# Kernel optimization log

Hardware: AMD Instinct MI355X
Metric: run time of the kernel (lower is better)

The kernel has to match this reference:

```python
import jax, jax.numpy as jnp
import numpy as np

B, S, D = 4, 2048, 1024  # batch, seq_len, d_emb (even for Givens pairs)


def givens_rotate(r, x):
    """Apply 2x2 Givens block rotations defined by r [D] to x [..., D]."""
    g = r.reshape(-1, 2)
    g = g / jnp.linalg.norm(g, axis=-1, keepdims=True)  # normalize (cos, sin) pairs
    xp = x.reshape(x.shape[:-1] + (x.shape[-1] // 2, 2))
    c, s = g[:, 0], g[:, 1]
    y0 = c * xp[..., 0] - s * xp[..., 1]
    y1 = c * xp[..., 1] + s * xp[..., 0]
    return jnp.stack([y0, y1], axis=-1).reshape(x.shape)


def setup_inputs() -> dict:
    key = jax.random.key(0)
    k1, k2 = jax.random.split(key, 2)
    Q = jax.random.normal(k1, (B, S, D), dtype=jnp.float32)
    # QKV_rotation.weight ~ U(-1, 1) per original init (before the identity overwrite)
    rot_w = jax.random.uniform(k2, (3, D), dtype=jnp.float32, minval=-1.0, maxval=1.0)
    scale = jnp.array([np.sqrt(D)], dtype=jnp.float32)
    bias = jnp.zeros((), dtype=jnp.float32)
    return {"Q": Q, "rot_w": rot_w, "scale": scale, "bias": bias}


def reference(Q, rot_w, scale, bias):
    # Givens-rotation 'projections' for q/k/v
    q = givens_rotate(rot_w[0], Q)
    k = givens_rotate(rot_w[1], Q)
    v = givens_rotate(rot_w[2], Q)
    # prepend zero time coordinate -> points on the Lorentz model ambient space
    zeros = jnp.zeros(Q.shape[:-1] + (1,), Q.dtype)
    q = jnp.concatenate([zeros, q], axis=-1)[:, None]  # [B,1,S,D+1]
    k = jnp.concatenate([zeros, k], axis=-1)[:, None]
    v = jnp.concatenate([zeros, v], axis=-1)[:, None]
    # Lorentz signature (-, +, +, ...)
    sgn = jnp.concatenate([-jnp.ones((1,), Q.dtype), jnp.ones((q.shape[-1] - 1,), Q.dtype)])
    # cinner(q, k): time-negated inner product -> scores [B,1,S,S]
    cin = jnp.einsum('bhqd,bhkd->bhqk', q * sgn, k)
    attn = jax.nn.softmax((2.0 + 2.0 * cin) / scale + bias, axis=-1)
    # Lorentz mid-point: weighted sum normalized by sqrt(|<m,m>_L|)
    ave = jnp.einsum('bhqk,bhkd->bhqd', attn, v)
    inner = jnp.sum(ave * ave * sgn, axis=-1, keepdims=True)
    denom = jnp.sqrt(jnp.clip(jnp.abs(inner), 1e-8, None))
    out = (ave / denom)[:, 0]  # [B,S,D+1]
    return out[..., 1:]  # drop time coordinate -> [B,S,D]
```

## Files before the change

kernel.cpp:

```cpp
#include <hip/hip_runtime.h>

typedef _Float16 h16;
typedef _Float16 half8 __attribute__((ext_vector_type(8)));
typedef float floatx4 __attribute__((ext_vector_type(4)));

static constexpr int Bb_ = 4, S_ = 2048, D_ = 1024;

static __device__ __forceinline__ void gl_lds16(const void* g, void* l) {
  __builtin_amdgcn_global_load_lds(
      (const __attribute__((address_space(1))) unsigned int*)g,
      (__attribute__((address_space(3))) unsigned int*)l, 16, 0, 0);
}

static __device__ __forceinline__ void rot_pair(float q0, float q1, float a0,
                                                float a1, float b0, float b1,
                                                float c0, float c1, float& y0,
                                                float& y1, float& v0,
                                                float& v1) {
  float iqk = rsqrtf((a0 * a0 + a1 * a1) * (b0 * b0 + b1 * b1));
  float cc = (a0 * b0 + a1 * b1) * iqk;
  float ss = (a0 * b1 - a1 * b0) * iqk;
  y0 = cc * q0 - ss * q1;
  y1 = cc * q1 + ss * q0;
  float iv = rsqrtf(c0 * c0 + c1 * c1);
  float cv = c0 * iv, sv = c1 * iv;
  v0 = cv * q0 - sv * q1;
  v1 = cv * q1 + sv * q0;
}

__global__ __launch_bounds__(256) void k_prep_t(
    const float* __restrict__ Q, const float* __restrict__ rot,
    h16* __restrict__ Qh, h16* __restrict__ Kh, h16* __restrict__ VhT,
    float* __restrict__ pss, unsigned int* __restrict__ flags) {
  __shared__ __align__(16) h16 tile[64][64];
  int d0 = blockIdx.x * 64, s0 = blockIdx.y * 64, b = blockIdx.z;
  int t = threadIdx.x;
  int bl = blockIdx.x + 16 * (blockIdx.y + 32 * blockIdx.z);
  if (flags && bl == 0 && t < 32) flags[t] = 0u;
  if (pss && t < 4) pss[bl * 4 + t] = 0.f;
  const float* Qb = Q + ((size_t)b * S_ + s0) * D_ + d0;
  h16* Qhb = Qh + ((size_t)b * S_ + s0) * D_ + d0;
  h16* Khb = Kh + ((size_t)b * S_ + s0) * D_ + d0;
#pragma unroll
  for (int i = 0; i < 2; ++i) {
    int c = t + 256 * i;
    int row = c >> 3;
    int col = (c & 7) * 8;
    float4 qa = *(const float4*)&Qb[(size_t)row * D_ + col];
    float4 qb = *(const float4*)&Qb[(size_t)row * D_ + col + 4];
    int dg = (d0 + col) >> 2;
    float4 r0a = ((const float4*)rot)[dg];
    float4 r0b = ((const float4*)rot)[dg + 1];
    float4 r1a = ((const float4*)rot)[D_ / 4 + dg];
    float4 r1b = ((const float4*)rot)[D_ / 4 + dg + 1];
    float4 r2a = ((const float4*)rot)[2 * D_ / 4 + dg];
    float4 r2b = ((const float4*)rot)[2 * D_ / 4 + dg + 1];
    float y0, y1, y2, y3, y4, y5, y6, y7;
    float v0, v1, v2, v3, v4, v5, v6, v7;
    rot_pair(qa.x, qa.y, r0a.x, r0a.y, r1a.x, r1a.y, r2a.x, r2a.y, y0, y1, v0, v1);
    rot_pair(qa.z, qa.w, r0a.z, r0a.w, r1a.z, r1a.w, r2a.z, r2a.w, y2, y3, v2, v3);
    rot_pair(qb.x, qb.y, r0b.x, r0b.y, r1b.x, r1b.y, r2b.x, r2b.y, y4, y5, v4, v5);
    rot_pair(qb.z, qb.w, r0b.z, r0b.w, r1b.z, r1b.w, r2b.z, r2b.w, y6, y7, v6, v7);
    half8 qh = {(h16)qa.x, (h16)qa.y, (h16)qa.z, (h16)qa.w,
                (h16)qb.x, (h16)qb.y, (h16)qb.z, (h16)qb.w};
    half8 kh = {(h16)y0, (h16)y1, (h16)y2, (h16)y3,
                (h16)y4, (h16)y5, (h16)y6, (h16)y7};
    half8 vh = {(h16)v0, (h16)v1, (h16)v2, (h16)v3,
                (h16)v4, (h16)v5, (h16)v6, (h16)v7};
    *(half8*)&Qhb[(size_t)row * D_ + col] = qh;
    *(half8*)&Khb[(size_t)row * D_ + col] = kh;
    int pcol = col ^ ((row >> 3) << 3);
    *(half8*)&tile[row][pcol] = vh;
  }
  __syncthreads();
  h16* dst = VhT + ((size_t)b * D_ + d0) * S_ + s0;
#pragma unroll
  for (int i = 0; i < 2; ++i) {
    int c = t + 256 * i;
    int drow = c >> 3;
    int sc = (c & 7) * 8;
    int xr = sc;
    half8 v;
#pragma unroll
    for (int j = 0; j < 8; ++j) v[j] = tile[sc + j][drow ^ xr];
    *(half8*)&dst[(size_t)drow * S_ + sc] = v;
  }
}

#define G_FENCE asm volatile("" ::: "memory")
#define G_BAR                     \
  do {                            \
    G_FENCE;                      \
    __builtin_amdgcn_s_barrier(); \
    G_FENCE;                      \
  } while (0)

template <int NF, bool OUT16>
__global__ __launch_bounds__(512, 2) void k_gemm8(
    const char* __restrict__ A, int a_pitch, unsigned long long a_batch,
    const char* __restrict__ Bt, int b_pitch, unsigned long long b_batch,
    void* __restrict__ C, int c_pitch, unsigned long long c_batch, int Kdim,
    const float* __restrict__ scale_p, float* __restrict__ pss,
    unsigned int* __restrict__ flags) {
  constexpr int BNR = NF * 64;
  constexpr int JQ = NF / 2;
  __shared__ __align__(16) h16 As[2][2][256 * 32];
  __shared__ __align__(16) h16 Bs[2][2][BNR * 32];
  const int t = threadIdx.x;
  const int lane = t & 63;
  const int w = t >> 6;
  const int wm = (w >> 2) * 128;
  const int wn = (w & 3) * (NF * 16);
  const int id = blockIdx.x + 8 * (blockIdx.y + 8 * blockIdx.z);
  const int L = (id & 7) * 32 + (id >> 3);
  const int tm = L & 7, tn = (L >> 3) & 7, tz = L >> 6;
  const int grp = tz * 8 + tm;
  const char* Ab = A + (unsigned long long)tz * a_batch +
                   (unsigned long long)(tm * 256) * (unsigned long long)a_pitch;
  const char* Bb = Bt + (unsigned long long)tz * b_batch +
                   (unsigned long long)(tn * BNR) * (unsigned long long)b_pitch;
  const int srow = t >> 2;
  const int scol = ((t & 3) ^ ((t >> 3) & 3)) << 4;
  const int lds_o = t * 16;
  const int mrow = lane & 15, kc = lane >> 4;
  const int koff = (kc ^ ((mrow >> 1) & 3)) << 3;
  const int NT = Kdim >> 6;

#define SG_A(bf, kt, hm)                                                  \
  do {                                                                    \
    const char* sp_ = Ab +                                                \
                      (unsigned long long)(srow + (hm) * 128) * a_pitch + \
                      (kt) * 128 + scol;                                  \
    gl_lds16(sp_, (char*)&As[bf][0][(hm) * 128 * 32] + lds_o);            \
    gl_lds16(sp_ + 64, (char*)&As[bf][1][(hm) * 128 * 32] + lds_o);       \
  } while (0)
#define SG_B(bf, kt, hm)                                                  \
  do {                                                                    \
    const char* sp_ = Bb +                                                \
                      (unsigned long long)(srow + (hm) * 128) * b_pitch + \
                      (kt) * 128 + scol;                                  \
    gl_lds16(sp_, (char*)&Bs[bf][0][(hm) * 128 * 32] + lds_o);            \
    gl_lds16(sp_ + 64, (char*)&Bs[bf][1][(hm) * 128 * 32] + lds_o);       \
  } while (0)

  half8 ar0[4][2], ar1[4][2], br0[JQ][2], br1[JQ][2];
  floatx4 acc[8][NF];
#pragma unroll
  for (int i = 0; i < 8; ++i)
#pragma unroll
    for (int j = 0; j < NF; ++j) acc[i][j] = (floatx4){0.f, 0.f, 0.f, 0.f};

#define LDA_(bf, mh, DST)                                                \
  do {                                                                   \
    _Pragma("unroll") for (int i_ = 0; i_ < 4; ++i_) {                   \
      DST[i_][0] = *(const half8*)&As[bf][0]                             \
                       [(wm + ((mh) * 4 + i_) * 16 + mrow) * 32 + koff]; \
      DST[i_][1] = *(const half8*)&As[bf][1]                             \
                       [(wm + ((mh) * 4 + i_) * 16 + mrow) * 32 + koff]; \
    }                                                                    \
  } while (0)
#define LDB_(bf, nh, DST)                                                \
  do {                                                                   \
    _Pragma("unroll") for (int j_ = 0; j_ < JQ; ++j_) {                  \
      DST[j_][0] = *(const half8*)&Bs[bf][0]                             \
                       [(wn + ((nh)*JQ + j_) * 16 + mrow) * 32 + koff];  \
      DST[j_][1] = *(const half8*)&Bs[bf][1]                             \
                       [(wn + ((nh)*JQ + j_) * 16 + mrow) * 32 + koff];  \
    }                                                                    \
  } while (0)
#define QUAD(mh, nh, AF, BF)                                                 \
  do {                                                                       \
    __builtin_amdgcn_s_setprio(1);                                           \
    _Pragma("unroll") for (int i_ = 0; i_ < 4; ++i_)                         \
        _Pragma("unroll") for (int j_ = 0; j_ < JQ; ++j_) {                  \
      acc[(mh) * 4 + i_][(nh)*JQ + j_] =                                     \
          __builtin_amdgcn_mfma_f32_16x16x32_f16(                            \
              AF[i_][0], BF[j_][0], acc[(mh) * 4 + i_][(nh)*JQ + j_], 0, 0,  \
              0);                                                            \
      acc[(mh) * 4 + i_][(nh)*JQ + j_] =                                     \
          __builtin_amdgcn_mfma_f32_16x16x32_f16(                            \
              AF[i_][1], BF[j_][1], acc[(mh) * 4 + i_][(nh)*JQ + j_], 0, 0,  \
              0);                                                            \
    }                                                                        \
    __builtin_amdgcn_s_setprio(0);                                           \
  } while (0)

  SG_A(0, 0, 0);
  SG_A(0, 0, 1);
  SG_B(0, 0, 0);
  if constexpr (NF == 4) SG_B(0, 0, 1);
  SG_B(1, 1, 0);
  if constexpr (NF == 4) SG_B(1, 1, 1);
  SG_A(1, 1, 0);
  if constexpr (NF == 4)
    asm volatile("s_waitcnt vmcnt(6)" ::: "memory");
  else
    asm volatile("s_waitcnt vmcnt(4)" ::: "memory");
  G_BAR;
  LDA_(0, 0, ar0);
  LDB_(0, 0, br0);

#define TILE_(bf, nb, u)                                   \
  do {                                                     \
    const int k1_ = ((u) + 1 < NT) ? (u) + 1 : NT - 1;     \
    const int k2_ = ((u) + 2 < NT) ? (u) + 2 : NT - 1;     \
                                                   \
    SG_A(nb, k1_, 1);                                      \
    G_BAR;                                                 \
    LDB_(bf, 1, br1);                                      \
    QUAD(0, 0, ar0, br0);                                  \
                                                   \
    G_BAR;                                                 \
    LDA_(bf, 1, ar1);                                      \
    QUAD(0, 1, ar0, br1);                                  \
                                                   \
    SG_B(bf, k2_, 0);                                      \
    G_BAR;                                                 \
    QUAD(1, 0, ar1, br0);                                  \
                                                   \
    if constexpr (NF == 4) SG_B(bf, k2_, 1);               \
    SG_A(bf, k2_, 0);                                      \
    if constexpr (NF == 4)                                 \
      asm volatile("s_waitcnt vmcnt(6)" ::: "memory");     \
    else                                                   \
      asm volatile("s_waitcnt vmcnt(4)" ::: "memory");     \
    G_BAR;                                                 \
    LDA_(nb, 0, ar0);  \
    LDB_(nb, 0, br0);                                      \
    QUAD(1, 1, ar1, br1);                                  \
  } while (0)

  for (int u = 0; u < NT; u += 2) {
    TILE_(0, 1, u);
    TILE_(1, 0, u + 1);
  }
  asm volatile("s_waitcnt vmcnt(0)" ::: "memory");

  const int m0 = tm * 256 + wm;
  const int n0 = tn * BNR + wn;
  const int ccol = lane & 15;
  const int rq = (lane >> 4) * 4;
  if constexpr (OUT16) {
    const float aexp = 2.0f / scale_p[0];
    h16* Cb = (h16*)C + (unsigned long long)tz * c_batch;
#pragma unroll
    for (int i = 0; i < 8; ++i)
#pragma unroll
      for (int j = 0; j < NF; ++j)
#pragma unroll
        for (int r = 0; r < 4; ++r)
          Cb[(unsigned long long)(m0 + i * 16 + rq + r) * c_pitch +
             (n0 + j * 16 + ccol)] = (h16)__expf(acc[i][j][r] * aexp - 8.0f);
  } else {
    float* Cb = (float*)C + (unsigned long long)tz * c_batch;
    if (pss) {
      __syncthreads();
      float* wsum = (float*)&As[0][0][0];
      float* finv = wsum + 4 * 256;
      float part[8][4];
#pragma unroll
      for (int i = 0; i < 8; ++i)
#pragma unroll
        for (int r = 0; r < 4; ++r) {
          float s = acc[i][0][r] * acc[i][0][r];
          if constexpr (NF > 1) s += acc[i][1][r] * acc[i][1][r];
#pragma unroll
          for (int m = 1; m < 16; m <<= 1) s += __shfl_xor(s, m);
          part[i][r] = s;
        }
      if ((lane & 15) == 0) {
#pragma unroll
        for (int i = 0; i < 8; ++i)
#pragma unroll
          for (int r = 0; r < 4; ++r)
            wsum[(w & 3) * 256 + wm + i * 16 + rq + r] = part[i][r];
      }
      __syncthreads();
      if (t < 256) {
        float s = wsum[t] + wsum[256 + t] + wsum[512 + t] + wsum[768 + t];
        __hip_atomic_fetch_add(&pss[(unsigned)grp * 256 + t], s,
                               __ATOMIC_RELAXED, __HIP_MEMORY_SCOPE_AGENT);
      }
      __syncthreads();
      if (t == 0) {
        __hip_atomic_fetch_add(&flags[grp], 1u, __ATOMIC_ACQ_REL,
                               __HIP_MEMORY_SCOPE_AGENT);
        while (__hip_atomic_load(&flags[grp], __ATOMIC_ACQUIRE,
                                 __HIP_MEMORY_SCOPE_AGENT) < 8u)
          __builtin_amdgcn_s_sleep(2);
      }
      __syncthreads();
      if (t < 256) {
        float ss2 = __hip_atomic_load(&pss[(unsigned)grp * 256 + t],
                                      __ATOMIC_RELAXED,
                                      __HIP_MEMORY_SCOPE_AGENT);
        finv[t] = rsqrtf(fmaxf(ss2, 1e-30f));
      }
      __syncthreads();
#pragma unroll
      for (int i = 0; i < 8; ++i) {
#pragma unroll
        for (int r = 0; r < 4; ++r) {
          const float f = finv[wm + i * 16 + rq + r];
#pragma unroll
          for (int j = 0; j < NF; ++j)
            Cb[(unsigned long long)(m0 + i * 16 + rq + r) * c_pitch +
               (n0 + j * 16 + ccol)] = acc[i][j][r] * f;
        }
      }
    } else {
#pragma unroll
      for (int i = 0; i < 8; ++i)
#pragma unroll
        for (int j = 0; j < NF; ++j)
#pragma unroll
          for (int r = 0; r < 4; ++r)
            Cb[(unsigned long long)(m0 + i * 16 + rq + r) * c_pitch +
               (n0 + j * 16 + ccol)] = acc[i][j][r];
    }
  }
#undef TILE_
#undef QUAD
#undef LDB_
#undef LDA_
#undef SG_B
#undef SG_A
}

__global__ __launch_bounds__(256) void k_epilogue(float* __restrict__ O) {
  int wv = threadIdx.x >> 6, ln = threadIdx.x & 63;
  int row = blockIdx.x * 4 + wv;
  float* base = O + (size_t)row * D_;
  float4 u[4];
#pragma unroll
  for (int r = 0; r < 4; ++r) u[r] = ((const float4*)base)[ln + 64 * r];
  float ss = 0.f;
#pragma unroll
  for (int r = 0; r < 4; ++r)
    ss += u[r].x * u[r].x + u[r].y * u[r].y + u[r].z * u[r].z + u[r].w * u[r].w;
#pragma unroll
  for (int off = 32; off; off >>= 1) ss += __shfl_xor(ss, off);
  float f = rsqrtf(fmaxf(ss, 1e-30f));
#pragma unroll
  for (int r = 0; r < 4; ++r) {
    float4 o;
    o.x = u[r].x * f;
    o.y = u[r].y * f;
    o.z = u[r].z * f;
    o.w = u[r].w * f;
    ((float4*)base)[ln + 64 * r] = o;
  }
}

extern "C" void kernel_launch(void* const* d_in, const int* in_sizes, int n_in,
                              void* d_out, int out_size, void* d_ws, size_t ws_size,
                              hipStream_t stream) {
  const float* Q = (const float*)d_in[0];
  const float* rot = (const float*)d_in[1];
  const float* scale = (const float*)d_in[2];
  float* O = (float*)d_out;
  char* ws = (char*)d_ws;
  const size_t MB = 1024ull * 1024ull;
  h16* Qh = (h16*)(ws);
  h16* Kh = (h16*)(ws + 16 * MB);
  h16* VhT = (h16*)(ws + 32 * MB);
  h16* Sl = (h16*)(ws + 48 * MB);
  float* pss = (float*)(ws + 80 * MB);
  unsigned int* flags = (unsigned int*)(ws + 80 * MB + 32 * 1024);
  const bool fused = ws_size >= 80 * MB + 32 * 1024 + 128;
  if (!fused) {
    pss = nullptr;
    flags = nullptr;
  }

  k_prep_t<<<dim3(D_ / 64, S_ / 64, Bb_), 256, 0, stream>>>(Q, rot, Qh, Kh,
                                                            VhT, pss, flags);
  k_gemm8<4, true><<<dim3(8, 8, 4), 512, 0, stream>>>(
      (const char*)Qh, D_ * 2, (unsigned long long)S_ * D_ * 2,
      (const char*)Kh, D_ * 2, (unsigned long long)S_ * D_ * 2,
      (void*)Sl, S_, (unsigned long long)S_ * S_, D_, scale, nullptr, nullptr);
  k_gemm8<2, false><<<dim3(8, 8, 4), 512, 0, stream>>>(
      (const char*)Sl, S_ * 2, (unsigned long long)S_ * S_ * 2,
      (const char*)VhT, S_ * 2, (unsigned long long)D_ * S_ * 2,
      (void*)O, D_, (unsigned long long)S_ * D_, S_, nullptr, pss, flags);
  if (!fused) k_epilogue<<<dim3(Bb_ * S_ / 4), 256, 0, stream>>>(O);
}
```

Before: 177.5 us.

## Halve GEMM block to 4 waves, each computing double-width output tile

```diff
diff --git a/kernel.cpp b/kernel.cpp
--- a/kernel.cpp
+++ b/kernel.cpp
@@ -96,21 +96,21 @@
   } while (0)
 
 template <int NF, bool OUT16>
-__global__ __launch_bounds__(512, 2) void k_gemm8(
+__global__ __launch_bounds__(256, 1) void k_gemm8(
     const char* __restrict__ A, int a_pitch, unsigned long long a_batch,
     const char* __restrict__ Bt, int b_pitch, unsigned long long b_batch,
     void* __restrict__ C, int c_pitch, unsigned long long c_batch, int Kdim,
     const float* __restrict__ scale_p, float* __restrict__ pss,
     unsigned int* __restrict__ flags) {
   constexpr int BNR = NF * 64;
-  constexpr int JQ = NF / 2;
+  constexpr int NW = NF * 2;
   __shared__ __align__(16) h16 As[2][2][256 * 32];
   __shared__ __align__(16) h16 Bs[2][2][BNR * 32];
   const int t = threadIdx.x;
   const int lane = t & 63;
   const int w = t >> 6;
-  const int wm = (w >> 2) * 128;
-  const int wn = (w & 3) * (NF * 16);
+  const int wm = (w >> 1) * 128;
+  const int wn = (w & 1) * (NF * 32);
   const int id = blockIdx.x + 8 * (blockIdx.y + 8 * blockIdx.z);
   const int L = (id & 7) * 32 + (id >> 3);
   const int tm = L & 7, tn = (L >> 3) & 7, tz = L >> 6;
@@ -119,36 +119,47 @@
                    (unsigned long long)(tm * 256) * (unsigned long long)a_pitch;
   const char* Bb = Bt + (unsigned long long)tz * b_batch +
                    (unsigned long long)(tn * BNR) * (unsigned long long)b_pitch;
-  const int srow = t >> 2;
-  const int scol = ((t & 3) ^ ((t >> 3) & 3)) << 4;
-  const int lds_o = t * 16;
+  const int o0 = t * 16, o1 = o0 + 4096;
+  const int r0_ = o0 >> 6, r1_ = o1 >> 6;
+  const int c0_ = ((((o0 >> 4) & 3) ^ ((r0_ >> 1) & 3)) << 4);
+  const int c1_ = ((((o1 >> 4) & 3) ^ ((r1_ >> 1) & 3)) << 4);
   const int mrow = lane & 15, kc = lane >> 4;
   const int koff = (kc ^ ((mrow >> 1) & 3)) << 3;
   const int NT = Kdim >> 6;
 
-#define SG_A(bf, kt, hm)                                                  \
-  do {                                                                    \
-    const char* sp_ = Ab +                                                \
-                      (unsigned long long)(srow + (hm) * 128) * a_pitch + \
-                      (kt) * 128 + scol;                                  \
-    gl_lds16(sp_, (char*)&As[bf][0][(hm) * 128 * 32] + lds_o);            \
-    gl_lds16(sp_ + 64, (char*)&As[bf][1][(hm) * 128 * 32] + lds_o);       \
-  } while (0)
-#define SG_B(bf, kt, hm)                                                  \
-  do {                                                                    \
-    const char* sp_ = Bb +                                                \
-                      (unsigned long long)(srow + (hm) * 128) * b_pitch + \
-                      (kt) * 128 + scol;                                  \
-    gl_lds16(sp_, (char*)&Bs[bf][0][(hm) * 128 * 32] + lds_o);            \
-    gl_lds16(sp_ + 64, (char*)&Bs[bf][1][(hm) * 128 * 32] + lds_o);       \
-  } while (0)
-
-  half8 ar0[4][2], ar1[4][2], br0[JQ][2], br1[JQ][2];
-  floatx4 acc[8][NF];
+#define SG_A(bf, kt, hm)                                                     \
+  do {                                                                       \
+    const char* pa_ = Ab +                                                   \
+                      (unsigned long long)(r0_ + (hm) * 128) * a_pitch +     \
+                      (kt) * 128;                                            \
+    const char* pb_ = Ab +                                                   \
+                      (unsigned long long)(r1_ + (hm) * 128) * a_pitch +     \
+                      (kt) * 128;                                            \
+    gl_lds16(pa_ + c0_, (char*)&As[bf][0][(hm) * 128 * 32] + o0);            \
+    gl_lds16(pa_ + c0_ + 64, (char*)&As[bf][1][(hm) * 128 * 32] + o0);       \
+    gl_lds16(pb_ + c1_, (char*)&As[bf][0][(hm) * 128 * 32] + o1);            \
+    gl_lds16(pb_ + c1_ + 64, (char*)&As[bf][1][(hm) * 128 * 32] + o1);       \
+  } while (0)
+#define SG_B(bf, kt, hm)                                                     \
+  do {                                                                       \
+    const char* pa_ = Bb +                                                   \
+                      (unsigned long long)(r0_ + (hm) * 128) * b_pitch +     \
+                      (kt) * 128;                                            \
+    const char* pb_ = Bb +                                                   \
+                      (unsigned long long)(r1_ + (hm) * 128) * b_pitch +     \
+                      (kt) * 128;                                            \
+    gl_lds16(pa_ + c0_, (char*)&Bs[bf][0][(hm) * 128 * 32] + o0);            \
+    gl_lds16(pa_ + c0_ + 64, (char*)&Bs[bf][1][(hm) * 128 * 32] + o0);       \
+    gl_lds16(pb_ + c1_, (char*)&Bs[bf][0][(hm) * 128 * 32] + o1);            \
+    gl_lds16(pb_ + c1_ + 64, (char*)&Bs[bf][1][(hm) * 128 * 32] + o1);       \
+  } while (0)
+
+  half8 ar0[4][2], ar1[4][2], br0[NF][2], br1[NF][2];
+  floatx4 acc[8][NW];
 #pragma unroll
   for (int i = 0; i < 8; ++i)
 #pragma unroll
-    for (int j = 0; j < NF; ++j) acc[i][j] = (floatx4){0.f, 0.f, 0.f, 0.f};
+    for (int j = 0; j < NW; ++j) acc[i][j] = (floatx4){0.f, 0.f, 0.f, 0.f};
 
 #define LDA_(bf, mh, DST)                                                \
   do {                                                                   \
@@ -161,25 +172,25 @@
   } while (0)
 #define LDB_(bf, nh, DST)                                                \
   do {                                                                   \
-    _Pragma("unroll") for (int j_ = 0; j_ < JQ; ++j_) {                  \
+    _Pragma("unroll") for (int j_ = 0; j_ < NF; ++j_) {                  \
       DST[j_][0] = *(const half8*)&Bs[bf][0]                             \
-                       [(wn + ((nh)*JQ + j_) * 16 + mrow) * 32 + koff];  \
+                       [(wn + ((nh)*NF + j_) * 16 + mrow) * 32 + koff];  \
       DST[j_][1] = *(const half8*)&Bs[bf][1]                             \
-                       [(wn + ((nh)*JQ + j_) * 16 + mrow) * 32 + koff];  \
+                       [(wn + ((nh)*NF + j_) * 16 + mrow) * 32 + koff];  \
     }                                                                    \
   } while (0)
 #define QUAD(mh, nh, AF, BF)                                                 \
   do {                                                                       \
     __builtin_amdgcn_s_setprio(1);                                           \
     _Pragma("unroll") for (int i_ = 0; i_ < 4; ++i_)                         \
-        _Pragma("unroll") for (int j_ = 0; j_ < JQ; ++j_) {                  \
-      acc[(mh) * 4 + i_][(nh)*JQ + j_] =                                     \
+        _Pragma("unroll") for (int j_ = 0; j_ < NF; ++j_) {                  \
+      acc[(mh) * 4 + i_][(nh)*NF + j_] =                                     \
           __builtin_amdgcn_mfma_f32_16x16x32_f16(                            \
-              AF[i_][0], BF[j_][0], acc[(mh) * 4 + i_][(nh)*JQ + j_], 0, 0,  \
+              AF[i_][0], BF[j_][0], acc[(mh) * 4 + i_][(nh)*NF + j_], 0, 0,  \
               0);                                                            \
-      acc[(mh) * 4 + i_][(nh)*JQ + j_] =                                     \
+      acc[(mh) * 4 + i_][(nh)*NF + j_] =                                     \
           __builtin_amdgcn_mfma_f32_16x16x32_f16(                            \
-              AF[i_][1], BF[j_][1], acc[(mh) * 4 + i_][(nh)*JQ + j_], 0, 0,  \
+              AF[i_][1], BF[j_][1], acc[(mh) * 4 + i_][(nh)*NF + j_], 0, 0,  \
               0);                                                            \
     }                                                                        \
     __builtin_amdgcn_s_setprio(0);                                           \
@@ -193,9 +204,9 @@
   if constexpr (NF == 4) SG_B(1, 1, 1);
   SG_A(1, 1, 0);
   if constexpr (NF == 4)
-    asm volatile("s_waitcnt vmcnt(6)" ::: "memory");
+    asm volatile("s_waitcnt vmcnt(12)" ::: "memory");
   else
-    asm volatile("s_waitcnt vmcnt(4)" ::: "memory");
+    asm volatile("s_waitcnt vmcnt(8)" ::: "memory");
   G_BAR;
   LDA_(0, 0, ar0);
   LDB_(0, 0, br0);
@@ -221,9 +232,9 @@
     if constexpr (NF == 4) SG_B(bf, k2_, 1);               \
     SG_A(bf, k2_, 0);                                      \
     if constexpr (NF == 4)                                 \
-      asm volatile("s_waitcnt vmcnt(6)" ::: "memory");     \
+      asm volatile("s_waitcnt vmcnt(12)" ::: "memory");    \
     else                                                   \
-      asm volatile("s_waitcnt vmcnt(4)" ::: "memory");     \
+      asm volatile("s_waitcnt vmcnt(8)" ::: "memory");     \
     G_BAR;                                                 \
     LDA_(nb, 0, ar0);  \
     LDB_(nb, 0, br0);                                      \
@@ -246,7 +257,7 @@
 #pragma unroll
     for (int i = 0; i < 8; ++i)
 #pragma unroll
-      for (int j = 0; j < NF; ++j)
+      for (int j = 0; j < NW; ++j)
 #pragma unroll
         for (int r = 0; r < 4; ++r)
           Cb[(unsigned long long)(m0 + i * 16 + rq + r) * c_pitch +
@@ -256,14 +267,15 @@
     if (pss) {
       __syncthreads();
       float* wsum = (float*)&As[0][0][0];
-      float* finv = wsum + 4 * 256;
+      float* finv = wsum + 2 * 256;
       float part[8][4];
 #pragma unroll
       for (int i = 0; i < 8; ++i)
 #pragma unroll
         for (int r = 0; r < 4; ++r) {
-          float s = acc[i][0][r] * acc[i][0][r];
-          if constexpr (NF > 1) s += acc[i][1][r] * acc[i][1][r];
+          float s = 0.f;
+#pragma unroll
+          for (int j = 0; j < NW; ++j) s += acc[i][j][r] * acc[i][j][r];
 #pragma unroll
           for (int m = 1; m < 16; m <<= 1) s += __shfl_xor(s, m);
           part[i][r] = s;
@@ -273,11 +285,11 @@
         for (int i = 0; i < 8; ++i)
 #pragma unroll
           for (int r = 0; r < 4; ++r)
-            wsum[(w & 3) * 256 + wm + i * 16 + rq + r] = part[i][r];
-      }
-      __syncthreads();
-      if (t < 256) {
-        float s = wsum[t] + wsum[256 + t] + wsum[512 + t] + wsum[768 + t];
+            wsum[(w & 1) * 256 + wm + i * 16 + rq + r] = part[i][r];
+      }
+      __syncthreads();
+      {
+        float s = wsum[t] + wsum[256 + t];
         __hip_atomic_fetch_add(&pss[(unsigned)grp * 256 + t], s,
                                __ATOMIC_RELAXED, __HIP_MEMORY_SCOPE_AGENT);
       }
@@ -290,7 +302,7 @@
           __builtin_amdgcn_s_sleep(2);
       }
       __syncthreads();
-      if (t < 256) {
+      {
         float ss2 = __hip_atomic_load(&pss[(unsigned)grp * 256 + t],
                                       __ATOMIC_RELAXED,
                                       __HIP_MEMORY_SCOPE_AGENT);
@@ -303,7 +315,7 @@
         for (int r = 0; r < 4; ++r) {
           const float f = finv[wm + i * 16 + rq + r];
 #pragma unroll
-          for (int j = 0; j < NF; ++j)
+          for (int j = 0; j < NW; ++j)
             Cb[(unsigned long long)(m0 + i * 16 + rq + r) * c_pitch +
                (n0 + j * 16 + ccol)] = acc[i][j][r] * f;
         }
@@ -312,7 +324,7 @@
 #pragma unroll
       for (int i = 0; i < 8; ++i)
 #pragma unroll
-        for (int j = 0; j < NF; ++j)
+        for (int j = 0; j < NW; ++j)
 #pragma unroll
           for (int r = 0; r < 4; ++r)
             Cb[(unsigned long long)(m0 + i * 16 + rq + r) * c_pitch +
@@ -375,11 +387,11 @@
 
   k_prep_t<<<dim3(D_ / 64, S_ / 64, Bb_), 256, 0, stream>>>(Q, rot, Qh, Kh,
                                                             VhT, pss, flags);
-  k_gemm8<4, true><<<dim3(8, 8, 4), 512, 0, stream>>>(
+  k_gemm8<4, true><<<dim3(8, 8, 4), 256, 0, stream>>>(
       (const char*)Qh, D_ * 2, (unsigned long long)S_ * D_ * 2,
       (const char*)Kh, D_ * 2, (unsigned long long)S_ * D_ * 2,
       (void*)Sl, S_, (unsigned long long)S_ * S_, D_, scale, nullptr, nullptr);
-  k_gemm8<2, false><<<dim3(8, 8, 4), 512, 0, stream>>>(
+  k_gemm8<2, false><<<dim3(8, 8, 4), 256, 0, stream>>>(
       (const char*)Sl, S_ * 2, (unsigned long long)S_ * S_ * 2,
       (const char*)VhT, S_ * 2, (unsigned long long)D_ * S_ * 2,
       (void*)O, D_, (unsigned long long)S_ * D_, S_, nullptr, pss, flags);
```

Result: slower. 208.5 us (+17.5%).
